# Optimization experiments

Measured on AMD Instinct MI355X. Metric: run time of the kernel, lower is better.

Reference implementation:

```python
import jax, jax.numpy as jnp
import numpy as np

H = 2048       # hidden_size
POOL = 4096    # latent_pooler_dim
EPS = 1e-6


def setup_inputs() -> dict:
    key = jax.random.key(0)
    ks = jax.random.split(key, 8)
    B, S = 16, 4096
    scale = 1.0 / np.sqrt(H)
    return {
        "last_hidden_states": jax.random.normal(ks[0], (B, S, H), dtype=jnp.float32),
        "attention_mask": jax.random.randint(ks[1], (B, S), 0, 2, dtype=jnp.int32),
        "latent_query": jax.random.normal(ks[2], (1, 1, H), dtype=jnp.float32),
        "Wq": jax.random.normal(ks[3], (H, H), dtype=jnp.float32) * scale,
        "Wk": jax.random.normal(ks[4], (H, H), dtype=jnp.float32) * scale,
        "Wv": jax.random.normal(ks[5], (H, H), dtype=jnp.float32) * scale,
        "Wo": jax.random.normal(ks[6], (POOL, H), dtype=jnp.float32) * scale,
        "norm_w": jnp.ones((H,), dtype=jnp.float32),
    }


def rms_norm(x, w, eps=EPS):
    xf = x.astype(jnp.float32)
    var = jnp.mean(xf * xf, axis=-1, keepdims=True)
    return w * (xf * jax.lax.rsqrt(var + eps)).astype(x.dtype)


def reference(last_hidden_states, attention_mask, latent_query, Wq, Wk, Wv, Wo, norm_w):
    B = last_hidden_states.shape[0]
    # single latent query per batch element: [B, H]
    q = jnp.broadcast_to(latent_query[0, 0], (B, H)) @ Wq.T            # [B, H]
    K = jnp.einsum('bsh,dh->bsd', last_hidden_states, Wk)               # [B, S, H]
    V = jnp.einsum('bsh,dh->bsd', last_hidden_states, Wv)               # [B, S, H]
    scores = jnp.einsum('bd,bsd->bs', q, K) / np.sqrt(H)                # [B, S]
    scores = jnp.where(attention_mask == 0, -jnp.inf, scores)
    weights = jax.nn.softmax(scores, axis=-1)                           # [B, S]
    pooled = jnp.einsum('bs,bsd->bd', weights, V)                       # [B, H]
    pooled = rms_norm(pooled, norm_w)
    return pooled @ Wo.T                                                # [B, POOL]
```

## Files before the change

kernel.cpp:

```cpp
#include <hip/hip_runtime.h>
#include <hip/hip_bf16.h>
#include <math.h>

#define H 2048
#define S 4096
#define B 16
#define POOL 4096
#define EPS 1e-6f
#define INV_SQRT_H 0.022097086912079608f

#define OFF_Q     0
#define OFF_QK    2048
#define OFF_NUM   4096
#define OFF_DEN   36864
#define OFF_PV    36880
#define OFF_NORM  69648

__device__ __forceinline__ float wave_reduce(float v) {
#pragma unroll
  for (int off = 32; off > 0; off >>= 1) v += __shfl_xor(v, off, 64);
  return v;
}

__global__ __launch_bounds__(256) void k_zero(float* __restrict__ p, int n) {
  int i = blockIdx.x * 256 + threadIdx.x;
  if (i < n) p[i] = 0.f;
}

__global__ __launch_bounds__(256) void k_q(const float* __restrict__ Wq,
                                           const float* __restrict__ lq,
                                           float* __restrict__ q) {
  const int d = blockIdx.x * 4 + (threadIdx.x >> 6);
  const int lane = threadIdx.x & 63;
  const float4* row = (const float4*)(Wq + (size_t)d * H);
  const float4* l4  = (const float4*)lq;
  float acc = 0.f;
#pragma unroll
  for (int k = 0; k < H / 4 / 64; ++k) {
    float4 w = row[lane + k * 64];
    float4 x = l4[lane + k * 64];
    acc += w.x * x.x + w.y * x.y + w.z * x.z + w.w * x.w;
  }
  acc = wave_reduce(acc);
  if (lane == 0) q[d] = acc;
}

__global__ __launch_bounds__(256) void k_qk(const float* __restrict__ Wk,
                                            const float* __restrict__ q,
                                            float* __restrict__ qk) {
  const int h  = blockIdx.x * 256 + threadIdx.x;
  const int d0 = blockIdx.y * 64;
  float local = 0.f;
#pragma unroll 8
  for (int dd = 0; dd < 64; ++dd) {
    local += q[d0 + dd] * Wk[(size_t)(d0 + dd) * H + h];
  }
  atomicAdd(&qk[h], local);
}

__global__ __launch_bounds__(256) void k_main(const float* __restrict__ X,
                                              const int* __restrict__ mask,
                                              const float* __restrict__ qk,
                                              float* __restrict__ num,
                                              float* __restrict__ den) {
  const int b  = blockIdx.y;
  const int s0 = blockIdx.x * 128;
  const int t  = threadIdx.x;
  const int c0 = t * 8;
  const int lane = t & 63;
  const int wv   = t >> 6;

  __shared__ float red[4][4];

  const float4 qa = *(const float4*)(qk + c0);
  const float4 qb = *(const float4*)(qk + c0 + 4);

  float acc[8];
#pragma unroll
  for (int j = 0; j < 8; ++j) acc[j] = 0.f;
  float denl = 0.f;

  const float* Xb = X + (size_t)b * S * H;
  const int*   mb = mask + b * S;

  for (int sb = 0; sb < 128; sb += 4) {
    float4 xa[4], xbv[4];
#pragma unroll
    for (int r = 0; r < 4; ++r) {
      const float* xp = Xb + (size_t)(s0 + sb + r) * H + c0;
      xa[r]  = *(const float4*)xp;
      xbv[r] = *(const float4*)(xp + 4);
      float p = xa[r].x * qa.x + xa[r].y * qa.y + xa[r].z * qa.z + xa[r].w * qa.w
              + xbv[r].x * qb.x + xbv[r].y * qb.y + xbv[r].z * qb.z + xbv[r].w * qb.w;
      p = wave_reduce(p);
      if (lane == 0) red[r][wv] = p;
    }
    __syncthreads();
#pragma unroll
    for (int r = 0; r < 4; ++r) {
      const int s = s0 + sb + r;
      float score = (red[r][0] + red[r][1] + red[r][2] + red[r][3]) * INV_SQRT_H;
      float w = mb[s] ? __expf(score) : 0.f;
      denl += w;
      acc[0] += w * xa[r].x;  acc[1] += w * xa[r].y;
      acc[2] += w * xa[r].z;  acc[3] += w * xa[r].w;
      acc[4] += w * xbv[r].x; acc[5] += w * xbv[r].y;
      acc[6] += w * xbv[r].z; acc[7] += w * xbv[r].w;
    }
    __syncthreads();
  }

#pragma unroll
  for (int j = 0; j < 8; ++j) atomicAdd(&num[b * H + c0 + j], acc[j]);
  if (t == 0) atomicAdd(&den[b], denl);
}

__global__ __launch_bounds__(256) void k_pv(const float* __restrict__ Wv,
                                            const float* __restrict__ num,
                                            const float* __restrict__ den,
                                            float* __restrict__ pv) {
  const int d = blockIdx.x * 4 + (threadIdx.x >> 6);
  const int lane = threadIdx.x & 63;
  const float4* wrow = (const float4*)(Wv + (size_t)d * H);
  const float4* n4   = (const float4*)num;
  float acc[B];
#pragma unroll
  for (int bb = 0; bb < B; ++bb) acc[bb] = 0.f;
  for (int k = lane; k < H / 4; k += 64) {
    float4 w = wrow[k];
#pragma unroll
    for (int bb = 0; bb < B; ++bb) {
      float4 v = n4[bb * (H / 4) + k];
      acc[bb] += w.x * v.x + w.y * v.y + w.z * v.z + w.w * v.w;
    }
  }
#pragma unroll
  for (int bb = 0; bb < B; ++bb) acc[bb] = wave_reduce(acc[bb]);
  if (lane == 0) {
#pragma unroll
    for (int bb = 0; bb < B; ++bb) pv[bb * H + d] = acc[bb] / den[bb];
  }
}

__global__ __launch_bounds__(256) void k_rms(const float* __restrict__ pv,
                                             const float* __restrict__ nw,
                                             float* __restrict__ normed) {
  const int b = blockIdx.x;
  const int t = threadIdx.x;
  __shared__ float sred[4];
  float ss = 0.f;
  for (int h = t; h < H; h += 256) {
    float v = pv[b * H + h];
    ss += v * v;
  }
  ss = wave_reduce(ss);
  if ((t & 63) == 0) sred[t >> 6] = ss;
  __syncthreads();
  float tot = sred[0] + sred[1] + sred[2] + sred[3];
  float sc = rsqrtf(tot / (float)H + EPS);
  for (int h = t; h < H; h += 256) normed[b * H + h] = pv[b * H + h] * sc * nw[h];
}

__global__ __launch_bounds__(256) void k_out(const float* __restrict__ Wo,
                                             const float* __restrict__ normed,
                                             float* __restrict__ out) {
  const int p = blockIdx.x * 4 + (threadIdx.x >> 6);
  const int lane = threadIdx.x & 63;
  const float4* wrow = (const float4*)(Wo + (size_t)p * H);
  const float4* n4   = (const float4*)normed;
  float acc[B];
#pragma unroll
  for (int bb = 0; bb < B; ++bb) acc[bb] = 0.f;
  for (int k = lane; k < H / 4; k += 64) {
    float4 w = wrow[k];
#pragma unroll
    for (int bb = 0; bb < B; ++bb) {
      float4 v = n4[bb * (H / 4) + k];
      acc[bb] += w.x * v.x + w.y * v.y + w.z * v.z + w.w * v.w;
    }
  }
#pragma unroll
  for (int bb = 0; bb < B; ++bb) acc[bb] = wave_reduce(acc[bb]);
  if (lane == 0) {
#pragma unroll
    for (int bb = 0; bb < B; ++bb) out[bb * POOL + p] = acc[bb];
  }
}

extern "C" void kernel_launch(void* const* d_in, const int* in_sizes, int n_in,
                              void* d_out, int out_size, void* d_ws, size_t ws_size,
                              hipStream_t stream) {
  (void)in_sizes; (void)n_in; (void)out_size; (void)ws_size;
  const float* X    = (const float*)d_in[0];
  const int*   mask = (const int*)d_in[1];
  const float* lq   = (const float*)d_in[2];
  const float* Wq   = (const float*)d_in[3];
  const float* Wk   = (const float*)d_in[4];
  const float* Wv   = (const float*)d_in[5];
  const float* Wo   = (const float*)d_in[6];
  const float* nw   = (const float*)d_in[7];
  float* out = (float*)d_out;
  float* ws  = (float*)d_ws;

  float* q      = ws + OFF_Q;
  float* qk     = ws + OFF_QK;
  float* num    = ws + OFF_NUM;
  float* den    = ws + OFF_DEN;
  float* pv     = ws + OFF_PV;
  float* normed = ws + OFF_NORM;

  {
    int n = OFF_PV - OFF_QK;
    k_zero<<<(n + 255) / 256, 256, 0, stream>>>(ws + OFF_QK, n);
  }
  k_q<<<H / 4, 256, 0, stream>>>(Wq, lq, q);
  k_qk<<<dim3(H / 256, 32), 256, 0, stream>>>(Wk, q, qk);
  k_main<<<dim3(S / 128, B), 256, 0, stream>>>(X, mask, qk, num, den);
  k_pv<<<H / 4, 256, 0, stream>>>(Wv, num, den, pv);
  k_rms<<<B, 256, 0, stream>>>(pv, nw, normed);
  k_out<<<POOL / 4, 256, 0, stream>>>(Wo, normed, out);
}
```

Before: 816.4 us.

## Skip masked rows per-wave in pooled attention and fuse zero/RMS kernels

The main kernel is restructured so each wave handles 32 whole rows independently, skipping rows whose mask is zero entirely (no load of X). This removes the per-4-row block syncs and roughly halves HBM traffic on X given the random mask. Partial sums are reduced through shared-memory atomics before global atomics. Separately, the zeroing kernel is folded into k_q and RMS norm is folded into k_pv (sum of squares) and k_out (scale), cutting two launches. The risk is more atomic traffic and wave divergence in the skip loop.

After: 781.6 us. -4.3%, faster.

```diff
diff --git a/kernel.cpp b/kernel.cpp
--- a/kernel.cpp
+++ b/kernel.cpp
@@ -13,8 +13,10 @@
 #define OFF_QK    2048
 #define OFF_NUM   4096
 #define OFF_DEN   36864
-#define OFF_PV    36880
-#define OFF_NORM  69648
+#define OFF_SSQ   36880
+#define OFF_PV    36896
+#define ZERO_BEG  OFF_QK
+#define ZERO_END  (OFF_SSQ + 16)
 
 __device__ __forceinline__ float wave_reduce(float v) {
 #pragma unroll
@@ -22,14 +24,13 @@
   return v;
 }
 
-__global__ __launch_bounds__(256) void k_zero(float* __restrict__ p, int n) {
-  int i = blockIdx.x * 256 + threadIdx.x;
-  if (i < n) p[i] = 0.f;
-}
-
 __global__ __launch_bounds__(256) void k_q(const float* __restrict__ Wq,
                                            const float* __restrict__ lq,
-                                           float* __restrict__ q) {
+                                           float* __restrict__ ws) {
+  {
+    int i = ZERO_BEG + blockIdx.x * 256 + threadIdx.x;
+    if (blockIdx.x < 137 && i < ZERO_END) ws[i] = 0.f;
+  }
   const int d = blockIdx.x * 4 + (threadIdx.x >> 6);
   const int lane = threadIdx.x & 63;
   const float4* row = (const float4*)(Wq + (size_t)d * H);
@@ -42,18 +43,18 @@
     acc += w.x * x.x + w.y * x.y + w.z * x.z + w.w * x.w;
   }
   acc = wave_reduce(acc);
-  if (lane == 0) q[d] = acc;
+  if (lane == 0) ws[OFF_Q + d] = acc;
 }
 
 __global__ __launch_bounds__(256) void k_qk(const float* __restrict__ Wk,
-                                            const float* __restrict__ q,
+                                            const float* __restrict__ ws_q,
                                             float* __restrict__ qk) {
   const int h  = blockIdx.x * 256 + threadIdx.x;
   const int d0 = blockIdx.y * 64;
   float local = 0.f;
 #pragma unroll 8
   for (int dd = 0; dd < 64; ++dd) {
-    local += q[d0 + dd] * Wk[(size_t)(d0 + dd) * H + h];
+    local += ws_q[d0 + dd] * Wk[(size_t)(d0 + dd) * H + h];
   }
   atomicAdd(&qk[h], local);
 }
@@ -66,61 +67,74 @@
   const int b  = blockIdx.y;
   const int s0 = blockIdx.x * 128;
   const int t  = threadIdx.x;
-  const int c0 = t * 8;
   const int lane = t & 63;
   const int wv   = t >> 6;
 
-  __shared__ float red[4][4];
-
-  const float4 qa = *(const float4*)(qk + c0);
-  const float4 qb = *(const float4*)(qk + c0 + 4);
-
-  float acc[8];
-#pragma unroll
-  for (int j = 0; j < 8; ++j) acc[j] = 0.f;
+  __shared__ float lnum[H];
+  __shared__ float lden;
+#pragma unroll
+  for (int j = 0; j < 8; ++j) lnum[t * 8 + j] = 0.f;
+  if (t == 0) lden = 0.f;
+
+  float4 qv[8];
+#pragma unroll
+  for (int k = 0; k < 8; ++k) qv[k] = *(const float4*)(qk + 4 * (lane + 64 * k));
+
+  float4 acc[8];
+#pragma unroll
+  for (int k = 0; k < 8; ++k) acc[k] = make_float4(0.f, 0.f, 0.f, 0.f);
   float denl = 0.f;
 
-  const float* Xb = X + (size_t)b * S * H;
-  const int*   mb = mask + b * S;
-
-  for (int sb = 0; sb < 128; sb += 4) {
-    float4 xa[4], xbv[4];
-#pragma unroll
-    for (int r = 0; r < 4; ++r) {
-      const float* xp = Xb + (size_t)(s0 + sb + r) * H + c0;
-      xa[r]  = *(const float4*)xp;
-      xbv[r] = *(const float4*)(xp + 4);
-      float p = xa[r].x * qa.x + xa[r].y * qa.y + xa[r].z * qa.z + xa[r].w * qa.w
-              + xbv[r].x * qb.x + xbv[r].y * qb.y + xbv[r].z * qb.z + xbv[r].w * qb.w;
-      p = wave_reduce(p);
-      if (lane == 0) red[r][wv] = p;
-    }
-    __syncthreads();
-#pragma unroll
-    for (int r = 0; r < 4; ++r) {
-      const int s = s0 + sb + r;
-      float score = (red[r][0] + red[r][1] + red[r][2] + red[r][3]) * INV_SQRT_H;
-      float w = mb[s] ? __expf(score) : 0.f;
-      denl += w;
-      acc[0] += w * xa[r].x;  acc[1] += w * xa[r].y;
-      acc[2] += w * xa[r].z;  acc[3] += w * xa[r].w;
-      acc[4] += w * xbv[r].x; acc[5] += w * xbv[r].y;
-      acc[6] += w * xbv[r].z; acc[7] += w * xbv[r].w;
-    }
-    __syncthreads();
-  }
-
-#pragma unroll
-  for (int j = 0; j < 8; ++j) atomicAdd(&num[b * H + c0 + j], acc[j]);
-  if (t == 0) atomicAdd(&den[b], denl);
+  const int srow0 = s0 + wv * 32;
+  const float* Xw = X + (size_t)b * S * H + (size_t)srow0 * H;
+  const int*   mb = mask + b * S + srow0;
+
+  __syncthreads();
+
+  for (int r = 0; r < 32; ++r) {
+    if (mb[r] == 0) continue;
+    const float* xp = Xw + (size_t)r * H;
+    float4 x[8];
+#pragma unroll
+    for (int k = 0; k < 8; ++k) x[k] = *(const float4*)(xp + 4 * (lane + 64 * k));
+    float p = 0.f;
+#pragma unroll
+    for (int k = 0; k < 8; ++k)
+      p += x[k].x * qv[k].x + x[k].y * qv[k].y + x[k].z * qv[k].z + x[k].w * qv[k].w;
+    p = wave_reduce(p);
+    float w = __expf(p * INV_SQRT_H);
+    denl += w;
+#pragma unroll
+    for (int k = 0; k < 8; ++k) {
+      acc[k].x += w * x[k].x; acc[k].y += w * x[k].y;
+      acc[k].z += w * x[k].z; acc[k].w += w * x[k].w;
+    }
+  }
+
+#pragma unroll
+  for (int k = 0; k < 8; ++k) {
+    const int c = 4 * (lane + 64 * k);
+    atomicAdd(&lnum[c + 0], acc[k].x);
+    atomicAdd(&lnum[c + 1], acc[k].y);
+    atomicAdd(&lnum[c + 2], acc[k].z);
+    atomicAdd(&lnum[c + 3], acc[k].w);
+  }
+  if (lane == 0) atomicAdd(&lden, denl);
+  __syncthreads();
+#pragma unroll
+  for (int j = 0; j < 8; ++j) atomicAdd(&num[b * H + t * 8 + j], lnum[t * 8 + j]);
+  if (t == 0) atomicAdd(&den[b], lden);
 }
 
 __global__ __launch_bounds__(256) void k_pv(const float* __restrict__ Wv,
                                             const float* __restrict__ num,
                                             const float* __restrict__ den,
-                                            float* __restrict__ pv) {
+                                            const float* __restrict__ nw,
+                                            float* __restrict__ pv,
+                                            float* __restrict__ ssq) {
   const int d = blockIdx.x * 4 + (threadIdx.x >> 6);
   const int lane = threadIdx.x & 63;
+  const int wv   = threadIdx.x >> 6;
   const float4* wrow = (const float4*)(Wv + (size_t)d * H);
   const float4* n4   = (const float4*)num;
   float acc[B];
@@ -136,38 +150,33 @@
   }
 #pragma unroll
   for (int bb = 0; bb < B; ++bb) acc[bb] = wave_reduce(acc[bb]);
+
+  __shared__ float sblk[4][B];
   if (lane == 0) {
-#pragma unroll
-    for (int bb = 0; bb < B; ++bb) pv[bb * H + d] = acc[bb] / den[bb];
-  }
-}
-
-__global__ __launch_bounds__(256) void k_rms(const float* __restrict__ pv,
-                                             const float* __restrict__ nw,
-                                             float* __restrict__ normed) {
-  const int b = blockIdx.x;
-  const int t = threadIdx.x;
-  __shared__ float sred[4];
-  float ss = 0.f;
-  for (int h = t; h < H; h += 256) {
-    float v = pv[b * H + h];
-    ss += v * v;
-  }
-  ss = wave_reduce(ss);
-  if ((t & 63) == 0) sred[t >> 6] = ss;
+    const float nwd = nw[d];
+#pragma unroll
+    for (int bb = 0; bb < B; ++bb) {
+      float p = acc[bb] / den[bb];
+      pv[bb * H + d] = p * nwd;
+      sblk[wv][bb] = p * p;
+    }
+  }
   __syncthreads();
-  float tot = sred[0] + sred[1] + sred[2] + sred[3];
-  float sc = rsqrtf(tot / (float)H + EPS);
-  for (int h = t; h < H; h += 256) normed[b * H + h] = pv[b * H + h] * sc * nw[h];
+  if (threadIdx.x < B) {
+    atomicAdd(&ssq[threadIdx.x],
+              sblk[0][threadIdx.x] + sblk[1][threadIdx.x] +
+              sblk[2][threadIdx.x] + sblk[3][threadIdx.x]);
+  }
 }
 
 __global__ __launch_bounds__(256) void k_out(const float* __restrict__ Wo,
-                                             const float* __restrict__ normed,
+                                             const float* __restrict__ pv,
+                                             const float* __restrict__ ssq,
                                              float* __restrict__ out) {
   const int p = blockIdx.x * 4 + (threadIdx.x >> 6);
   const int lane = threadIdx.x & 63;
   const float4* wrow = (const float4*)(Wo + (size_t)p * H);
-  const float4* n4   = (const float4*)normed;
+  const float4* n4   = (const float4*)pv;
   float acc[B];
 #pragma unroll
   for (int bb = 0; bb < B; ++bb) acc[bb] = 0.f;
@@ -183,7 +192,10 @@
   for (int bb = 0; bb < B; ++bb) acc[bb] = wave_reduce(acc[bb]);
   if (lane == 0) {
 #pragma unroll
-    for (int bb = 0; bb < B; ++bb) out[bb * POOL + p] = acc[bb];
+    for (int bb = 0; bb < B; ++bb) {
+      float sc = rsqrtf(ssq[bb] * (1.0f / (float)H) + EPS);
+      out[bb * POOL + p] = acc[bb] * sc;
+    }
   }
 }
 
@@ -202,21 +214,11 @@
   float* out = (float*)d_out;
   float* ws  = (float*)d_ws;
 
-  float* q      = ws + OFF_Q;
-  float* qk     = ws + OFF_QK;
-  float* num    = ws + OFF_NUM;
-  float* den    = ws + OFF_DEN;
-  float* pv     = ws + OFF_PV;
-  float* normed = ws + OFF_NORM;
-
-  {
-    int n = OFF_PV - OFF_QK;
-    k_zero<<<(n + 255) / 256, 256, 0, stream>>>(ws + OFF_QK, n);
-  }
-  k_q<<<H / 4, 256, 0, stream>>>(Wq, lq, q);
-  k_qk<<<dim3(H / 256, 32), 256, 0, stream>>>(Wk, q, qk);
-  k_main<<<dim3(S / 128, B), 256, 0, stream>>>(X, mask, qk, num, den);
-  k_pv<<<H / 4, 256, 0, stream>>>(Wv, num, den, pv);
-  k_rms<<<B, 256, 0, stream>>>(pv, nw, normed);
-  k_out<<<POOL / 4, 256, 0, stream>>>(Wo, normed, out);
-}
+  k_q   <<<H / 4, 256, 0, stream>>>(Wq, lq, ws);
+  k_qk  <<<dim3(H / 256, 32), 256, 0, stream>>>(Wk, ws + OFF_Q, ws + OFF_QK);
+  k_main<<<dim3(S / 128, B), 256, 0, stream>>>(X, mask, ws + OFF_QK,
+                                               ws + OFF_NUM, ws + OFF_DEN);
+  k_pv  <<<H / 4, 256, 0, stream>>>(Wv, ws + OFF_NUM, ws + OFF_DEN, nw,
+                                    ws + OFF_PV, ws + OFF_SSQ);
+  k_out <<<POOL / 4, 256, 0, stream>>>(Wo, ws + OFF_PV, ws + OFF_SSQ, out);
+}
```
